# Kernel optimization log

Measured on AMD Instinct MI355X. Metric: run time of the kernel, lower is better.

The kernel has to match this reference:

```python
import jax, jax.numpy as jnp
import numpy as np

ROPE_BASE = 10000.0

def rotary_pe_3d(x, coords):
    # x: [B, H, L, D]; coords: [B, L, 3]. Split D into 3 axis chunks; rotate
    # each chunk (half-split pairs) by angles coord_axis * inv_freq.
    D = x.shape[-1]
    da = D // 3            # dims per spatial axis
    p = da // 2            # rotary pairs per axis
    inv_freq = 1.0 / (ROPE_BASE ** (jnp.arange(p, dtype=x.dtype) / p))  # [p]
    chunks = []
    for a in range(3):
        xa = x[..., a * da:(a + 1) * da]                       # [B,H,L,da]
        theta = coords[..., a][:, None, :, None] * inv_freq    # [B,1,L,p]
        cos, sin = jnp.cos(theta), jnp.sin(theta)
        x1, x2 = xa[..., :p], xa[..., p:]
        chunks.append(jnp.concatenate([x1 * cos - x2 * sin,
                                       x1 * sin + x2 * cos], axis=-1))
    if 3 * da < D:  # leave any remainder un-rotated
        chunks.append(x[..., 3 * da:])
    return jnp.concatenate(chunks, axis=-1)


def setup_inputs() -> dict:
    key = jax.random.key(0)
    ks = jax.random.split(key, 16)
    B, Lq, Lk, D, H = 4, 1024, 4096, 768, 8
    s = 1.0 / np.sqrt(D)
    return {
        "query": jax.random.normal(ks[0], (B, Lq, D), jnp.float32),
        "key": jax.random.normal(ks[1], (B, Lk, D), jnp.float32),
        "value": jax.random.normal(ks[2], (B, Lk, D), jnp.float32),
        "coords_query": jax.random.normal(ks[3], (B, Lq, 3), jnp.float32),
        "coords_key": jax.random.normal(ks[4], (B, Lk, 3), jnp.float32),
        "Wq": jax.random.normal(ks[5], (D, D), jnp.float32) * s,
        "bq": jnp.zeros((D,), jnp.float32),
        "Wk": jax.random.normal(ks[6], (D, D), jnp.float32) * s,
        "bk": jnp.zeros((D,), jnp.float32),
        "Wv": jax.random.normal(ks[7], (D, D), jnp.float32) * s,
        "bv": jnp.zeros((D,), jnp.float32),
        "Wo": jax.random.normal(ks[8], (D, D), jnp.float32) * s,
        "bo": jnp.zeros((D,), jnp.float32),
    }


def reference(query, key, value, coords_query, coords_key,
              Wq, bq, Wk, bk, Wv, bv, Wo, bo):
    B, Lq, D = query.shape
    Lk = key.shape[1]
    H = 8
    hd = D // H
    # Projections (nn.Linear: x @ W.T + b)
    q = (query @ Wq.T + bq).reshape(B, Lq, H, hd).transpose(0, 2, 1, 3)  # [B,H,Lq,hd]
    k = (key @ Wk.T + bk).reshape(B, Lk, H, hd).transpose(0, 2, 1, 3)
    v = (value @ Wv.T + bv).reshape(B, Lk, H, hd).transpose(0, 2, 1, 3)
    q = rotary_pe_3d(q, coords_query)
    k = rotary_pe_3d(k, coords_key)
    scores = jnp.einsum("bhqd,bhkd->bhqk", q, k) / jnp.sqrt(jnp.asarray(hd, q.dtype))
    attn = jax.nn.softmax(scores, axis=-1)  # dropout is identity in eval
    out = jnp.einsum("bhqk,bhkd->bhqd", attn, v)
    out = out.transpose(0, 2, 1, 3).reshape(B, Lq, D)
    return out @ Wo.T + bo
```

## Files before the change

### kernel.cpp

```cpp
#include <hip/hip_runtime.h>
#include <math.h>

#define DM 768
#define NH 8
#define HD 96
#define BQ 4
#define LQ 1024
#define LK 4096
#define BH (BQ*NH)
#define KVS 4
#define KC (LK/KVS)
#define NT (KC/64)
#define QB 128
#define NW (DM*DM)
#define NKSTEP (DM/64)

typedef unsigned short ushort;
typedef unsigned int uint;
typedef __attribute__((ext_vector_type(8))) short short8v;
typedef __attribute__((ext_vector_type(4))) float float4v;

#define QSCALE 0.14724444641f

static __device__ __forceinline__ ushort f2bf(float x) {
    union { float f; uint u; } c; c.f = x;
    uint u = c.u;
    u += ((u >> 16) & 1u) + 0x7fffu;
    return (ushort)(u >> 16);
}

static __device__ __forceinline__ float bf2f(ushort x) {
    union { uint u; float f; } c; c.u = (uint)x << 16;
    return c.f;
}

static __device__ __forceinline__ uint cvtpk(float lo, float hi) {
    uint d;
    asm("v_cvt_pk_bf16_f32 %0, %1, %2" : "=v"(d) : "v"(lo), "v"(hi));
    return d;
}

static __device__ __forceinline__ float exp2hw(float x) {
#if __has_builtin(__builtin_amdgcn_exp2f)
    return __builtin_amdgcn_exp2f(x);
#else
    return __expf(x * 0.6931471805599453f);
#endif
}

static __device__ __forceinline__ void gload_lds16(const void* g, void* l) {
    __builtin_amdgcn_global_load_lds(
        (const __attribute__((address_space(1))) uint*)g,
        (__attribute__((address_space(3))) uint*)l, 16, 0, 0);
}

__global__ __launch_bounds__(256)
void wcvt(const float* __restrict__ w0, const float* __restrict__ w1,
          const float* __restrict__ w2, const float* __restrict__ w3,
          ushort* __restrict__ d)
{
    const int SEG = NW / 1024;
    int b = blockIdx.x;
    int wsel = b / SEG, ib = b % SEG;
    const float* s = (wsel == 0) ? w0 : (wsel == 1) ? w1 : (wsel == 2) ? w2 : w3;
    int i = ib * 256 + threadIdx.x;
    float4 v = ((const float4*)s)[i];
    uint2 o;
    o.x = (uint)f2bf(v.x) | ((uint)f2bf(v.y) << 16);
    o.y = (uint)f2bf(v.z) | ((uint)f2bf(v.w) << 16);
    ((uint2*)(d + (size_t)wsel * NW))[i] = o;
}

__global__ __launch_bounds__(256, 3)
void qkv_gemm(const float* __restrict__ qf, const float* __restrict__ kf,
              const float* __restrict__ vf,
              const ushort* __restrict__ wqb, const ushort* __restrict__ wkb,
              const ushort* __restrict__ wvb,
              const float* __restrict__ bq, const float* __restrict__ bk,
              const float* __restrict__ bv,
              const float* __restrict__ cq, const float* __restrict__ ck,
              ushort* __restrict__ qws, ushort* __restrict__ kws,
              ushort* __restrict__ vtb)
{
    __shared__ ushort Sh[24576];
    char* As = (char*)Sh;
    char* Bs = (char*)Sh + 32768;

    const int tid  = threadIdx.x;
    const int w    = tid >> 6;
    const int lane = tid & 63;
    const int l15  = lane & 15;
    const int lg   = lane >> 4;
    const int wm   = w >> 1, wn = w & 1;

    const int L = blockIdx.x;
    int seg, idx, Lshift, rpx;
    const float* X32; const ushort* Wbp; const float* bias; const float* coords;
    ushort* out; float oscale;
    if (L < 192)      { seg = 0; idx = L;       X32 = qf; Wbp = wqb; bias = bq; coords = cq; out = qws; Lshift = 10; rpx = 4;  oscale = QSCALE; }
    else if (L < 960) { seg = 1; idx = L - 192; X32 = kf; Wbp = wkb; bias = bk; coords = ck; out = kws; Lshift = 12; rpx = 16; oscale = 1.0f; }
    else              { seg = 2; idx = L - 960; X32 = vf; Wbp = wvb; bias = bv; coords = 0;  out = vtb; Lshift = 12; rpx = 16; oscale = 1.0f; }

    const int xcd  = idx & 7;
    const int sq   = idx >> 3;
    const int col0 = (sq % 6) * 128;
    const int row0 = (xcd * rpx + sq / 6) * 128;

    float4v acc[4][4];
    #pragma unroll
    for (int m = 0; m < 4; ++m)
        #pragma unroll
        for (int n = 0; n < 4; ++n) acc[m][n] = (float4v)0.f;

    int PA[8], rA[8], cA[8];
    #pragma unroll
    for (int c = 0; c < 8; ++c) {
        int P = ((w*8 + c) << 10) + lane*16;
        int r = P >> 8;
        int j = ((P >> 4) & 15) ^ (r & 15);
        PA[c] = P;
        rA[c] = r;
        cA[c] = j * 4;
    }
    int PB[4], rB[4], cB[4];
    #pragma unroll
    for (int c = 0; c < 4; ++c) {
        int P = ((w*4 + c) << 10) + lane*16;
        int lgc = P ^ (((P >> 9) & 3) << 5);
        PB[c] = P;
        rB[c] = lgc >> 7;
        cB[c] = (lgc & 127) >> 1;
    }
    const float*  xb = X32 + (size_t)row0 * DM;
    const ushort* wb = Wbp + (size_t)col0 * DM;

    int offA0[2][4], offA1[2][4], offB[2][4];
    #pragma unroll
    for (int kk = 0; kk < 2; ++kk) {
        #pragma unroll
        for (int m = 0; m < 4; ++m) {
            int R  = wm*64 + m*16 + l15;
            int j0 = kk*8 + lg*2;
            offA0[kk][m] = R*256 + (((j0    ) ^ (R & 15)) << 4);
            offA1[kk][m] = R*256 + (((j0 + 1) ^ (R & 15)) << 4);
            int byte = (wn*64 + m*16 + l15)*128 + kk*64 + lg*16;
            offB[kk][m] = byte ^ (((byte >> 9) & 3) << 5);
        }
    }

    for (int kt = 0; kt < DM; kt += 64) {
        #pragma unroll
        for (int c = 0; c < 8; ++c)
            gload_lds16(xb + (size_t)rA[c]*DM + kt + cA[c], As + PA[c]);
        #pragma unroll
        for (int c = 0; c < 4; ++c)
            gload_lds16(wb + (size_t)rB[c]*DM + kt + cB[c], Bs + PB[c]);
        __syncthreads();
        #pragma unroll
        for (int kk = 0; kk < 2; ++kk) {
            short8v af[4], bfm[4];
            #pragma unroll
            for (int m = 0; m < 4; ++m) {
                float4 x0 = *(const float4*)(As + offA0[kk][m]);
                float4 x1 = *(const float4*)(As + offA1[kk][m]);
                union { uint4 u; short8v s; } cv;
                cv.u.x = cvtpk(x0.x, x0.y);
                cv.u.y = cvtpk(x0.z, x0.w);
                cv.u.z = cvtpk(x1.x, x1.y);
                cv.u.w = cvtpk(x1.z, x1.w);
                af[m] = cv.s;
            }
            #pragma unroll
            for (int n = 0; n < 4; ++n)
                bfm[n] = *(const short8v*)(Bs + offB[kk][n]);
            #pragma unroll
            for (int m = 0; m < 4; ++m)
                #pragma unroll
                for (int n = 0; n < 4; ++n)
                    acc[m][n] = __builtin_amdgcn_mfma_f32_16x16x32_bf16(af[m], bfm[n], acc[m][n], 0, 0, 0);
        }
        __syncthreads();
    }

    const int colbase = col0 + wn*64;
    float bvv[4];
    #pragma unroll
    for (int nt = 0; nt < 4; ++nt) bvv[nt] = bias[colbase + nt*16 + l15];
    #pragma unroll
    for (int m = 0; m < 4; ++m)
        #pragma unroll
        for (int nt = 0; nt < 4; ++nt)
            #pragma unroll
            for (int r = 0; r < 4; ++r) acc[m][nt][r] += bvv[nt];

    if (seg < 2) {
        const float freq = exp2f(-(float)l15 * 0.83048202372184058696f);
        const int a0 = ((colbase >> 5) + 0) % 3;
        const int a1 = ((colbase >> 5) + 1) % 3;
        const int F  = (colbase >> 4) & 1;
        #pragma unroll
        for (int m = 0; m < 4; ++m) {
            #pragma unroll
            for (int r = 0; r < 4; ++r) {
                int row = row0 + wm*64 + m*16 + lg*4 + r;
                const float* c3 = coords + (size_t)row * 3;
                float sn0, cs0, sn1, cs1;
                __sincosf(c3[a0] * freq, &sn0, &cs0);
                __sincosf(c3[a1] * freq, &sn1, &cs1);
                {
                    float A_ = F ? acc[m][1][r] : acc[m][0][r];
                    float B_ = F ? acc[m][0][r] : acc[m][1][r];
                    float x1 = (A_*cs0 - B_*sn0) * oscale, x2 = (A_*sn0 + B_*cs0) * oscale;
                    if (F) { acc[m][1][r] = x1; acc[m][0][r] = x2; }
                    else   { acc[m][0][r] = x1; acc[m][1][r] = x2; }
                }
                {
                    float A_ = F ? acc[m][3][r] : acc[m][2][r];
                    float B_ = F ? acc[m][2][r] : acc[m][3][r];
                    float x1 = (A_*cs1 - B_*sn1) * oscale, x2 = (A_*sn1 + B_*cs1) * oscale;
                    if (F) { acc[m][3][r] = x1; acc[m][2][r] = x2; }
                    else   { acc[m][2][r] = x1; acc[m][3][r] = x2; }
                }
            }
        }
        const int Lm1 = (1 << Lshift) - 1;
        int hh[4], tt[4];
        #pragma unroll
        for (int nt = 0; nt < 4; ++nt) {
            int j0 = colbase + nt*16;
            hh[nt] = j0 / HD;
            tt[nt] = j0 % HD + l15;
        }
        #pragma unroll
        for (int m = 0; m < 4; ++m)
            #pragma unroll
            for (int r = 0; r < 4; ++r) {
                int row = row0 + wm*64 + m*16 + lg*4 + r;
                int b = row >> Lshift, l = row & Lm1;
                #pragma unroll
                for (int nt = 0; nt < 4; ++nt)
                    out[(((size_t)b*NH + hh[nt]) << Lshift | l) * HD + tt[nt]] =
                        f2bf(acc[m][nt][r]);
            }
    } else {
        #pragma unroll
        for (int m = 0; m < 4; ++m)
            #pragma unroll
            for (int nt = 0; nt < 4; ++nt)
                #pragma unroll
                for (int r = 0; r < 4; ++r) {
                    int c  = wn*64 + nt*16 + l15;
                    int ri = wm*64 + m*16 + lg*4 + r;
                    *(ushort*)(As + c*256 + (((ri>>3) ^ (c&7))<<4) + (ri&7)*2)
                        = f2bf(acc[m][nt][r]);
                }
        __syncthreads();
        #pragma unroll
        for (int e = 0; e < 8; ++e) {
            int idx2 = tid + 256*e;
            int c = idx2 >> 4, r8 = idx2 & 15;
            uint4 val = *(const uint4*)(As + c*256 + ((r8 ^ (c&7))<<4));
            int j = col0 + c;
            int h = j / HD, t = j % HD;
            int row = row0 + r8*8;
            int b = row >> 12, l = row & (LK-1);
            *(uint4*)&out[(((size_t)b*NH + h)*HD + t)*LK + l] = val;
        }
    }
}

__global__ __launch_bounds__(256)
void gemm_out(const ushort* __restrict__ X, const ushort* __restrict__ Wb,
              const float* __restrict__ bias, float* __restrict__ out)
{
    __shared__ ushort Sh[16384];
    ushort* As = Sh;
    ushort* Bs = Sh + 8192;

    const int tid  = threadIdx.x;
    const int w    = tid >> 6;
    const int lane = tid & 63;
    const int l15  = lane & 15;
    const int lg   = lane >> 4;
    const int wm   = w >> 1, wn = w & 1;

    const int L    = blockIdx.x;
    const int xcd  = L & 7;
    const int sq   = L >> 3;
    const int col0 = (sq % 6) * 128;
    const int row0 = (xcd * 4 + sq / 6) * 128;

    float4v acc[4][4];
    #pragma unroll
    for (int m = 0; m < 4; ++m)
        #pragma unroll
        for (int n = 0; n < 4; ++n) acc[m][n] = (float4v)0.f;

    int Pp[4], rrS[4], cbS[4];
    #pragma unroll
    for (int c = 0; c < 4; ++c) {
        int P = ((w*4 + c) << 10) + lane*16;
        int lgc = P ^ (((P >> 9) & 3) << 5);
        Pp[c]  = P;
        rrS[c] = lgc >> 7;
        cbS[c] = (lgc & 127) >> 1;
    }
    const ushort* xb = X  + (size_t)row0 * DM;
    const ushort* wb = Wb + (size_t)col0 * DM;

    int offA[2][4], offB[2][4];
    #pragma unroll
    for (int kk = 0; kk < 2; ++kk) {
        #pragma unroll
        for (int m = 0; m < 4; ++m) {
            int byte = (wm*64 + m*16 + l15)*128 + kk*64 + lg*16;
            offA[kk][m] = byte ^ (((byte >> 9) & 3) << 5);
            byte = (wn*64 + m*16 + l15)*128 + kk*64 + lg*16;
            offB[kk][m] = byte ^ (((byte >> 9) & 3) << 5);
        }
    }

    for (int kt = 0; kt < DM; kt += 64) {
        #pragma unroll
        for (int c = 0; c < 4; ++c) {
            gload_lds16(xb + (size_t)rrS[c]*DM + kt + cbS[c], (char*)As + Pp[c]);
            gload_lds16(wb + (size_t)rrS[c]*DM + kt + cbS[c], (char*)Bs + Pp[c]);
        }
        __syncthreads();
        #pragma unroll
        for (int kk = 0; kk < 2; ++kk) {
            short8v af[4], bfm[4];
            #pragma unroll
            for (int m = 0; m < 4; ++m)
                af[m] = *(const short8v*)((const char*)As + offA[kk][m]);
            #pragma unroll
            for (int n = 0; n < 4; ++n)
                bfm[n] = *(const short8v*)((const char*)Bs + offB[kk][n]);
            #pragma unroll
            for (int m = 0; m < 4; ++m)
                #pragma unroll
                for (int n = 0; n < 4; ++n)
                    acc[m][n] = __builtin_amdgcn_mfma_f32_16x16x32_bf16(af[m], bfm[n], acc[m][n], 0, 0, 0);
        }
        __syncthreads();
    }

    const int colbase = col0 + wn*64;
    float bvv[4];
    #pragma unroll
    for (int nt = 0; nt < 4; ++nt) bvv[nt] = bias[colbase + nt*16 + l15];
    #pragma unroll
    for (int m = 0; m < 4; ++m)
        #pragma unroll
        for (int r = 0; r < 4; ++r) {
            int row = row0 + wm*64 + m*16 + lg*4 + r;
            #pragma unroll
            for (int nt = 0; nt < 4; ++nt)
                out[(size_t)row*DM + colbase + nt*16 + l15] = acc[m][nt][r] + bvv[nt];
        }
}

__global__ __launch_bounds__(256, 2)
void attn_mfma(const ushort* __restrict__ q, const ushort* __restrict__ k,
               const ushort* __restrict__ vt, ushort* __restrict__ opb,
               float* __restrict__ mlb)
{
    __shared__ ushort Ks[64*128];
    __shared__ ushort Vs[96*64];
    __shared__ ushort PsT[4][32][72];

    const int tid  = threadIdx.x;
    const int w    = tid >> 6;
    const int lane = tid & 63;
    const int l15  = lane & 15;
    const int lg   = lane >> 4;

    const int L   = blockIdx.x;
    const int xcd = L & 7;
    const int s   = L >> 3;
    const int pr  = xcd*16 + (s >> 3);
    const int qt  = s & 7;
    const int bh  = pr & 31;
    const int sc  = pr >> 5;

    const ushort* qg = q  + ((size_t)bh * LQ + qt*QB + w*32 + l15) * HD;
    const ushort* kg = k  + ((size_t)bh * LK + (size_t)sc * KC) * HD;
    const ushort* vg = vt + (size_t)bh * HD * LK + (size_t)sc * KC;

    short8v aq0[3], aq1[3];
    #pragma unroll
    for (int dc = 0; dc < 3; ++dc) {
        aq0[dc] = *(const short8v*)(qg + dc*32 + lg*8);
        aq1[dc] = *(const short8v*)(qg + 16*HD + dc*32 + lg*8);
    }

    int kdst[3], ksrc[3], vdst[3], vsrc[3];
    #pragma unroll
    for (int j = 0; j < 3; ++j) {
        int c = tid + 256*j;
        int kr = c / 12, ks = c % 12;
        kdst[j] = kr*256 + ((ks ^ (kr & 7)) << 4);
        ksrc[j] = kr*HD + ks*8;
        int vr = c >> 3, vs = c & 7;
        vdst[j] = vr*128 + ((vs ^ (vr & 7)) << 4);
        vsrc[j] = vr*LK + vs*8;
    }
    int tK[3], tV[2];
    #pragma unroll
    for (int dc = 0; dc < 3; ++dc) tK[dc] = ((dc*4 + lg) ^ (l15 & 7)) << 4;
    #pragma unroll
    for (int h2 = 0; h2 < 2; ++h2)  tV[h2] = ((h2*4 + lg) ^ (l15 & 7)) << 4;

    float4v o0[6], o1[6];
    #pragma unroll
    for (int dt = 0; dt < 6; ++dt) { o0[dt] = (float4v)0.f; o1[dt] = (float4v)0.f; }
    float m_0 = -1e30f, l_0 = 0.f;
    float m_1 = -1e30f, l_1 = 0.f;

    short8v kreg[3], vreg[3];
    #pragma unroll
    for (int j = 0; j < 3; ++j) {
        kreg[j] = *(const short8v*)(kg + ksrc[j]);
        vreg[j] = *(const short8v*)(vg + vsrc[j]);
    }
    #pragma unroll
    for (int j = 0; j < 3; ++j) {
        *(short8v*)((char*)Ks + kdst[j]) = kreg[j];
        *(short8v*)((char*)Vs + vdst[j]) = vreg[j];
    }
    __syncthreads();

    for (int t = 0; t < NT; ++t) {
        if (t + 1 < NT) {
            const ushort* kn = kg + (size_t)(t+1)*64*HD;
            const ushort* vn = vg + (t+1)*64;
            #pragma unroll
            for (int j = 0; j < 3; ++j) {
                kreg[j] = *(const short8v*)(kn + ksrc[j]);
                vreg[j] = *(const short8v*)(vn + vsrc[j]);
            }
        }

        float4v s0[4], s1[4];
        __builtin_amdgcn_s_setprio(1);
        #pragma unroll
        for (int nt = 0; nt < 4; ++nt) {
            s0[nt] = (float4v)0.f;
            s1[nt] = (float4v)0.f;
            #pragma unroll
            for (int dc = 0; dc < 3; ++dc) {
                short8v bk = *(const short8v*)((const char*)Ks + nt*4096 + l15*256 + tK[dc]);
                s0[nt] = __builtin_amdgcn_mfma_f32_16x16x32_bf16(bk, aq0[dc], s0[nt], 0, 0, 0);
                s1[nt] = __builtin_amdgcn_mfma_f32_16x16x32_bf16(bk, aq1[dc], s1[nt], 0, 0, 0);
            }
        }
        __builtin_amdgcn_s_setprio(0);

        float mt0 = -1e30f, mt1 = -1e30f;
        #pragma unroll
        for (int nt = 0; nt < 4; ++nt)
            #pragma unroll
            for (int r = 0; r < 4; ++r) {
                mt0 = fmaxf(mt0, s0[nt][r]);
                mt1 = fmaxf(mt1, s1[nt][r]);
            }
        mt0 = fmaxf(mt0, __shfl_xor(mt0, 16, 64));
        mt0 = fmaxf(mt0, __shfl_xor(mt0, 32, 64));
        mt1 = fmaxf(mt1, __shfl_xor(mt1, 16, 64));
        mt1 = fmaxf(mt1, __shfl_xor(mt1, 32, 64));

        if (__any((mt0 > m_0 + 11.5f) || (mt1 > m_1 + 11.5f))) {
            float mn0 = fmaxf(m_0, mt0), mn1 = fmaxf(m_1, mt1);
            float a0 = exp2hw(m_0 - mn0), a1 = exp2hw(m_1 - mn1);
            m_0 = mn0; m_1 = mn1;
            l_0 *= a0;  l_1 *= a1;
            float al0[4], al1[4];
            #pragma unroll
            for (int r = 0; r < 4; ++r) {
                al0[r] = __shfl(a0, lg*4 + r, 64);
                al1[r] = __shfl(a1, lg*4 + r, 64);
            }
            #pragma unroll
            for (int dt = 0; dt < 6; ++dt)
                #pragma unroll
                for (int r = 0; r < 4; ++r) {
                    o0[dt][r] *= al0[r];
                    o1[dt][r] *= al1[r];
                }
        }

        float ps0 = 0.f, ps1 = 0.f;
        #pragma unroll
        for (int nt = 0; nt < 4; ++nt)
            #pragma unroll
            for (int r = 0; r < 4; ++r) {
                float p0 = exp2hw(s0[nt][r] - m_0);
                float p1 = exp2hw(s1[nt][r] - m_1);
                s0[nt][r] = p0; ps0 += p0;
                s1[nt][r] = p1; ps1 += p1;
            }
        ps0 += __shfl_xor(ps0, 16, 64);
        ps0 += __shfl_xor(ps0, 32, 64);
        ps1 += __shfl_xor(ps1, 16, 64);
        ps1 += __shfl_xor(ps1, 32, 64);
        l_0 += ps0;
        l_1 += ps1;

        #pragma unroll
        for (int nt = 0; nt < 4; ++nt) {
            uint2 pk0, pk1;
            pk0.x = cvtpk(s0[nt][0], s0[nt][1]);
            pk0.y = cvtpk(s0[nt][2], s0[nt][3]);
            pk1.x = cvtpk(s1[nt][0], s1[nt][1]);
            pk1.y = cvtpk(s1[nt][2], s1[nt][3]);
            *(uint2*)&PsT[w][l15][nt*16 + lg*4]      = pk0;
            *(uint2*)&PsT[w][16 + l15][nt*16 + lg*4] = pk1;
        }

        short8v a00 = *(const short8v*)&PsT[w][l15][lg*8];
        short8v a01 = *(const short8v*)&PsT[w][l15][32 + lg*8];
        short8v a10 = *(const short8v*)&PsT[w][16 + l15][lg*8];
        short8v a11 = *(const short8v*)&PsT[w][16 + l15][32 + lg*8];
        __builtin_amdgcn_s_setprio(1);
        #pragma unroll
        for (int dt = 0; dt < 6; ++dt) {
            short8v bv0 = *(const short8v*)((const char*)Vs + dt*2048 + l15*128 + tV[0]);
            short8v bv1 = *(const short8v*)((const char*)Vs + dt*2048 + l15*128 + tV[1]);
            o0[dt] = __builtin_amdgcn_mfma_f32_16x16x32_bf16(a00, bv0, o0[dt], 0, 0, 0);
            o0[dt] = __builtin_amdgcn_mfma_f32_16x16x32_bf16(a01, bv1, o0[dt], 0, 0, 0);
            o1[dt] = __builtin_amdgcn_mfma_f32_16x16x32_bf16(a10, bv0, o1[dt], 0, 0, 0);
            o1[dt] = __builtin_amdgcn_mfma_f32_16x16x32_bf16(a11, bv1, o1[dt], 0, 0, 0);
        }
        __builtin_amdgcn_s_setprio(0);
        __syncthreads();

        if (t + 1 < NT) {
            #pragma unroll
            for (int j = 0; j < 3; ++j) {
                *(short8v*)((char*)Ks + kdst[j]) = kreg[j];
                *(short8v*)((char*)Vs + vdst[j]) = vreg[j];
            }
        }
        __syncthreads();
    }

    ushort* ob = opb + (((size_t)sc * BH + bh) * LQ + qt*QB + w*32) * HD;
    #pragma unroll
    for (int r = 0; r < 4; ++r) {
        #pragma unroll
        for (int dt = 0; dt < 6; ++dt) {
            ob[(size_t)(lg*4 + r) * HD + dt*16 + l15]      = f2bf(o0[dt][r]);
            ob[(size_t)(16 + lg*4 + r) * HD + dt*16 + l15] = f2bf(o1[dt][r]);
        }
    }
    if (lane < 16) {
        size_t mlrow = ((size_t)sc * BH + bh) * LQ + qt*QB + w*32 + lane;
        mlb[mlrow*2 + 0] = m_0;
        mlb[mlrow*2 + 1] = l_0;
        mlb[(mlrow + 16)*2 + 0] = m_1;
        mlb[(mlrow + 16)*2 + 1] = l_1;
    }
}

__global__ __launch_bounds__(256)
void combine(const ushort* __restrict__ opb, const float* __restrict__ mlb,
             ushort* __restrict__ ctx)
{
    const int NROW = BH * LQ;
    int idx = blockIdx.x * 256 + threadIdx.x;
    int row = idx / 12, seg = idx % 12;

    float m[KVS], lv[KVS];
    #pragma unroll
    for (int i = 0; i < KVS; ++i) {
        m[i]  = mlb[((size_t)i*NROW + row)*2 + 0];
        lv[i] = mlb[((size_t)i*NROW + row)*2 + 1];
    }
    float ms = m[0];
    #pragma unroll
    for (int i = 1; i < KVS; ++i) ms = fmaxf(ms, m[i]);
    float wsum = 0.f, wgt[KVS];
    #pragma unroll
    for (int i = 0; i < KVS; ++i) {
        wgt[i] = exp2hw(m[i] - ms);
        wsum += lv[i] * wgt[i];
    }
    float inv = 1.f / wsum;

    float acc[8] = {};
    #pragma unroll
    for (int i = 0; i < KVS; ++i) {
        uint4 v = *(const uint4*)&opb[((size_t)i*NROW + row)*HD + seg*8];
        uint vv[4] = {v.x, v.y, v.z, v.w};
        #pragma unroll
        for (int j2 = 0; j2 < 4; ++j2) {
            acc[j2*2+0] += bf2f((ushort)(vv[j2] & 0xffff)) * wgt[i];
            acc[j2*2+1] += bf2f((ushort)(vv[j2] >> 16))    * wgt[i];
        }
    }

    int bh = row / LQ, l = row % LQ;
    int b = bh >> 3, h = bh & 7;
    ushort* o = ctx + ((size_t)b * LQ + l) * DM + h * HD + seg*8;
    uint4 pk;
    pk.x = cvtpk(acc[0]*inv, acc[1]*inv);
    pk.y = cvtpk(acc[2]*inv, acc[3]*inv);
    pk.z = cvtpk(acc[4]*inv, acc[5]*inv);
    pk.w = cvtpk(acc[6]*inv, acc[7]*inv);
    *(uint4*)o = pk;
}

extern "C" void kernel_launch(void* const* d_in, const int* in_sizes, int n_in,
                              void* d_out, int out_size, void* d_ws, size_t ws_size,
                              hipStream_t stream)
{
    const float* query = (const float*)d_in[0];
    const float* key   = (const float*)d_in[1];
    const float* value = (const float*)d_in[2];
    const float* cq    = (const float*)d_in[3];
    const float* ck    = (const float*)d_in[4];
    const float* Wq    = (const float*)d_in[5];
    const float* bqv   = (const float*)d_in[6];
    const float* Wk    = (const float*)d_in[7];
    const float* bkv   = (const float*)d_in[8];
    const float* Wv    = (const float*)d_in[9];
    const float* bvv   = (const float*)d_in[10];
    const float* Wo    = (const float*)d_in[11];
    const float* bov   = (const float*)d_in[12];
    float* out = (float*)d_out;

    const size_t NQ = (size_t)BQ * LQ * DM;
    const size_t NK = (size_t)BQ * LK * DM;
    const size_t NP = (size_t)KVS * BH * LQ * HD;

    ushort* wq  = (ushort*)d_ws;
    ushort* wk  = wq  + NW;
    ushort* wv  = wk  + NW;
    ushort* wo  = wv  + NW;
    ushort* qws = wo  + NW;
    ushort* kws = qws + NQ;
    ushort* vtb = kws + NK;
    ushort* opb = vtb + NK;
    ushort* ctx = opb + NP;
    float*  mlb = (float*)(ctx + NQ);

    wcvt<<<4*(NW/1024), 256, 0, stream>>>(Wq, Wk, Wv, Wo, wq);
    qkv_gemm<<<1728, 256, 0, stream>>>(query, key, value, wq, wk, wv,
                                       bqv, bkv, bvv, cq, ck, qws, kws, vtb);
    attn_mfma<<<(LQ/QB) * BH * KVS, 256, 0, stream>>>(qws, kws, vtb, opb, mlb);
    combine<<<BH*LQ*12/256, 256, 0, stream>>>(opb, mlb, ctx);
    gemm_out<<<(BQ*LQ/128)*6, 256, 0, stream>>>(ctx, wo, bov, out);
}
```

Measured before the change: 172.7 us.

## Load GEMM A-operand fragments directly from global memory into registers, bypassing LDS

In both the QKV projection GEMM and the output projection GEMM, the activation (A) tile is no longer staged through shared memory. Each lane reads its MFMA fragment straight from global memory into registers, and only the weight (B) tile stays in LDS. This halves or more the shared-memory footprint, which should allow higher occupancy (gemm_out now declares launch bounds of 3 blocks), and removes LDS write/read traffic. The cost is that the two warps sharing a row block now read the same A data redundantly from global memory, with less coalesced access and more register pressure for holding fp32 fragments.

```diff
diff --git a/kernel.cpp b/kernel.cpp
--- a/kernel.cpp
+++ b/kernel.cpp
@@ -82,9 +82,8 @@
               ushort* __restrict__ qws, ushort* __restrict__ kws,
               ushort* __restrict__ vtb)
 {
-    __shared__ ushort Sh[24576];
-    char* As = (char*)Sh;
-    char* Bs = (char*)Sh + 32768;
+    __shared__ ushort Sh[16384];
+    char* Bs = (char*)Sh;
 
     const int tid  = threadIdx.x;
     const int w    = tid >> 6;
@@ -112,16 +111,6 @@
         #pragma unroll
         for (int n = 0; n < 4; ++n) acc[m][n] = (float4v)0.f;
 
-    int PA[8], rA[8], cA[8];
-    #pragma unroll
-    for (int c = 0; c < 8; ++c) {
-        int P = ((w*8 + c) << 10) + lane*16;
-        int r = P >> 8;
-        int j = ((P >> 4) & 15) ^ (r & 15);
-        PA[c] = P;
-        rA[c] = r;
-        cA[c] = j * 4;
-    }
     int PB[4], rB[4], cB[4];
     #pragma unroll
     for (int c = 0; c < 4; ++c) {
@@ -134,40 +123,44 @@
     const float*  xb = X32 + (size_t)row0 * DM;
     const ushort* wb = Wbp + (size_t)col0 * DM;
 
-    int offA0[2][4], offA1[2][4], offB[2][4];
-    #pragma unroll
-    for (int kk = 0; kk < 2; ++kk) {
-        #pragma unroll
-        for (int m = 0; m < 4; ++m) {
-            int R  = wm*64 + m*16 + l15;
-            int j0 = kk*8 + lg*2;
-            offA0[kk][m] = R*256 + (((j0    ) ^ (R & 15)) << 4);
-            offA1[kk][m] = R*256 + (((j0 + 1) ^ (R & 15)) << 4);
-            int byte = (wn*64 + m*16 + l15)*128 + kk*64 + lg*16;
-            offB[kk][m] = byte ^ (((byte >> 9) & 3) << 5);
-        }
-    }
+    size_t aoff[4];
+    #pragma unroll
+    for (int m = 0; m < 4; ++m)
+        aoff[m] = (size_t)(wm*64 + m*16 + l15) * DM;
+
+    int offB[2][4];
+    #pragma unroll
+    for (int kk = 0; kk < 2; ++kk)
+        #pragma unroll
+        for (int n = 0; n < 4; ++n) {
+            int byte = (wn*64 + n*16 + l15)*128 + kk*64 + lg*16;
+            offB[kk][n] = byte ^ (((byte >> 9) & 3) << 5);
+        }
 
     for (int kt = 0; kt < DM; kt += 64) {
-        #pragma unroll
-        for (int c = 0; c < 8; ++c)
-            gload_lds16(xb + (size_t)rA[c]*DM + kt + cA[c], As + PA[c]);
         #pragma unroll
         for (int c = 0; c < 4; ++c)
             gload_lds16(wb + (size_t)rB[c]*DM + kt + cB[c], Bs + PB[c]);
+        float4 fa[2][4][2];
+        #pragma unroll
+        for (int kk = 0; kk < 2; ++kk)
+            #pragma unroll
+            for (int m = 0; m < 4; ++m) {
+                const float* src = xb + aoff[m] + kt + kk*32 + lg*8;
+                fa[kk][m][0] = *(const float4*)src;
+                fa[kk][m][1] = *(const float4*)(src + 4);
+            }
         __syncthreads();
         #pragma unroll
         for (int kk = 0; kk < 2; ++kk) {
             short8v af[4], bfm[4];
             #pragma unroll
             for (int m = 0; m < 4; ++m) {
-                float4 x0 = *(const float4*)(As + offA0[kk][m]);
-                float4 x1 = *(const float4*)(As + offA1[kk][m]);
                 union { uint4 u; short8v s; } cv;
-                cv.u.x = cvtpk(x0.x, x0.y);
-                cv.u.y = cvtpk(x0.z, x0.w);
-                cv.u.z = cvtpk(x1.x, x1.y);
-                cv.u.w = cvtpk(x1.z, x1.w);
+                cv.u.x = cvtpk(fa[kk][m][0].x, fa[kk][m][0].y);
+                cv.u.y = cvtpk(fa[kk][m][0].z, fa[kk][m][0].w);
+                cv.u.z = cvtpk(fa[kk][m][1].x, fa[kk][m][1].y);
+                cv.u.w = cvtpk(fa[kk][m][1].z, fa[kk][m][1].w);
                 af[m] = cv.s;
             }
             #pragma unroll
@@ -251,7 +244,7 @@
                 for (int r = 0; r < 4; ++r) {
                     int c  = wn*64 + nt*16 + l15;
                     int ri = wm*64 + m*16 + lg*4 + r;
-                    *(ushort*)(As + c*256 + (((ri>>3) ^ (c&7))<<4) + (ri&7)*2)
+                    *(ushort*)((char*)Sh + c*256 + (((ri>>3) ^ (c&7))<<4) + (ri&7)*2)
                         = f2bf(acc[m][nt][r]);
                 }
         __syncthreads();
@@ -259,7 +252,7 @@
         for (int e = 0; e < 8; ++e) {
             int idx2 = tid + 256*e;
             int c = idx2 >> 4, r8 = idx2 & 15;
-            uint4 val = *(const uint4*)(As + c*256 + ((r8 ^ (c&7))<<4));
+            uint4 val = *(const uint4*)((const char*)Sh + c*256 + ((r8 ^ (c&7))<<4));
             int j = col0 + c;
             int h = j / HD, t = j % HD;
             int row = row0 + r8*8;
@@ -269,13 +262,12 @@
     }
 }
 
-__global__ __launch_bounds__(256)
+__global__ __launch_bounds__(256, 3)
 void gemm_out(const ushort* __restrict__ X, const ushort* __restrict__ Wb,
               const float* __restrict__ bias, float* __restrict__ out)
 {
-    __shared__ ushort Sh[16384];
-    ushort* As = Sh;
-    ushort* Bs = Sh + 8192;
+    __shared__ ushort Sh[8192];
+    char* Bs = (char*)Sh;
 
     const int tid  = threadIdx.x;
     const int w    = tid >> 6;
@@ -296,51 +288,54 @@
         #pragma unroll
         for (int n = 0; n < 4; ++n) acc[m][n] = (float4v)0.f;
 
-    int Pp[4], rrS[4], cbS[4];
+    int PB[4], rB[4], cB[4];
     #pragma unroll
     for (int c = 0; c < 4; ++c) {
         int P = ((w*4 + c) << 10) + lane*16;
         int lgc = P ^ (((P >> 9) & 3) << 5);
-        Pp[c]  = P;
-        rrS[c] = lgc >> 7;
-        cbS[c] = (lgc & 127) >> 1;
+        PB[c] = P;
+        rB[c] = lgc >> 7;
+        cB[c] = (lgc & 127) >> 1;
     }
     const ushort* xb = X  + (size_t)row0 * DM;
     const ushort* wb = Wb + (size_t)col0 * DM;
 
-    int offA[2][4], offB[2][4];
-    #pragma unroll
-    for (int kk = 0; kk < 2; ++kk) {
-        #pragma unroll
-        for (int m = 0; m < 4; ++m) {
-            int byte = (wm*64 + m*16 + l15)*128 + kk*64 + lg*16;
-            offA[kk][m] = byte ^ (((byte >> 9) & 3) << 5);
-            byte = (wn*64 + m*16 + l15)*128 + kk*64 + lg*16;
-            offB[kk][m] = byte ^ (((byte >> 9) & 3) << 5);
-        }
-    }
+    size_t aoff[4];
+    #pragma unroll
+    for (int m = 0; m < 4; ++m)
+        aoff[m] = (size_t)(wm*64 + m*16 + l15) * DM;
+
+    int offB[2][4];
+    #pragma unroll
+    for (int kk = 0; kk < 2; ++kk)
+        #pragma unroll
+        for (int n = 0; n < 4; ++n) {
+            int byte = (wn*64 + n*16 + l15)*128 + kk*64 + lg*16;
+            offB[kk][n] = byte ^ (((byte >> 9) & 3) << 5);
+        }
 
     for (int kt = 0; kt < DM; kt += 64) {
         #pragma unroll
-        for (int c = 0; c < 4; ++c) {
-            gload_lds16(xb + (size_t)rrS[c]*DM + kt + cbS[c], (char*)As + Pp[c]);
-            gload_lds16(wb + (size_t)rrS[c]*DM + kt + cbS[c], (char*)Bs + Pp[c]);
-        }
+        for (int c = 0; c < 4; ++c)
+            gload_lds16(wb + (size_t)rB[c]*DM + kt + cB[c], Bs + PB[c]);
+        short8v afr[2][4];
+        #pragma unroll
+        for (int kk = 0; kk < 2; ++kk)
+            #pragma unroll
+            for (int m = 0; m < 4; ++m)
+                afr[kk][m] = *(const short8v*)(xb + aoff[m] + kt + kk*32 + lg*8);
         __syncthreads();
         #pragma unroll
         for (int kk = 0; kk < 2; ++kk) {
-            short8v af[4], bfm[4];
-            #pragma unroll
-            for (int m = 0; m < 4; ++m)
-                af[m] = *(const short8v*)((const char*)As + offA[kk][m]);
+            short8v bfm[4];
             #pragma unroll
             for (int n = 0; n < 4; ++n)
-                bfm[n] = *(const short8v*)((const char*)Bs + offB[kk][n]);
+                bfm[n] = *(const short8v*)(Bs + offB[kk][n]);
             #pragma unroll
             for (int m = 0; m < 4; ++m)
                 #pragma unroll
                 for (int n = 0; n < 4; ++n)
-                    acc[m][n] = __builtin_amdgcn_mfma_f32_16x16x32_bf16(af[m], bfm[n], acc[m][n], 0, 0, 0);
+                    acc[m][n] = __builtin_amdgcn_mfma_f32_16x16x32_bf16(afr[kk][m], bfm[n], acc[m][n], 0, 0, 0);
         }
         __syncthreads();
     }
```

Measured after the change: 275.9 us. +59.7%, slower.
